# Kernel tuning notes

Measured on AMD Instinct MI355X. Metric: run time of the kernel, lower is better.

The kernel has to match this reference:

```python
import jax, jax.numpy as jnp
import numpy as np

NUM_NODES = 50000
NODE_DIM = 32
EDGE_DIM = 7
HIDDEN_DIM = 64
NUM_EDGES = 200000


def setup_inputs() -> dict:
    key = jax.random.key(0)
    ks = jax.random.split(key, 12)
    s = lambda *d: 1.0 / np.sqrt(d[0])
    return {
        "edge_index": jax.random.randint(ks[0], (2, NUM_EDGES), 0, NUM_NODES, dtype=jnp.int64)
        if jax.config.jax_enable_x64 else jax.random.randint(ks[0], (2, NUM_EDGES), 0, NUM_NODES, dtype=jnp.int32),
        "edge_attr": jax.random.normal(ks[1], (NUM_EDGES, EDGE_DIM), dtype=jnp.float32),
        # learned parameters
        "node_emb": jax.random.normal(ks[2], (NUM_NODES, NODE_DIM), dtype=jnp.float32),
        "w_nn": jax.random.normal(ks[3], (EDGE_DIM, NODE_DIM * HIDDEN_DIM), dtype=jnp.float32) * s(EDGE_DIM),
        "b_nn": jnp.zeros((NODE_DIM * HIDDEN_DIM,), dtype=jnp.float32),
        "root_w": jax.random.normal(ks[4], (NODE_DIM, HIDDEN_DIM), dtype=jnp.float32) * s(NODE_DIM),
        "conv_bias": jnp.zeros((HIDDEN_DIM,), dtype=jnp.float32),
        "w_e1": jax.random.normal(ks[5], (2 * HIDDEN_DIM + EDGE_DIM, 64), dtype=jnp.float32) * s(2 * HIDDEN_DIM + EDGE_DIM),
        "b_e1": jnp.zeros((64,), dtype=jnp.float32),
        "w_e2": jax.random.normal(ks[6], (64, 2), dtype=jnp.float32) * s(64),
        "b_e2": jnp.zeros((2,), dtype=jnp.float32),
    }


def reference(edge_index, edge_attr, node_emb, w_nn, b_nn, root_w, conv_bias,
              w_e1, b_e1, w_e2, b_e2):
    src, dst = edge_index[0], edge_index[1]
    x = node_emb  # [N, node_dim]
    # NNConv: per-edge weight matrix from edge MLP (Linear + ReLU)
    w_edge = jax.nn.relu(edge_attr @ w_nn + b_nn).reshape(-1, NODE_DIM, HIDDEN_DIM)  # [E, in, out]
    # gather source features, per-edge matmul, scatter-add to dst (aggr='add')
    msg = jnp.einsum("ei,eio->eo", x[src], w_edge)  # [E, hidden]
    agg = jax.ops.segment_sum(msg, dst, num_segments=NUM_NODES)  # [N, hidden]
    h = jax.nn.relu(agg + x @ root_w + conv_bias)  # conv root term + bias, then outer ReLU
    # edge classifier MLP
    edge_repr = jnp.concatenate([h[src], h[dst], edge_attr], axis=1)  # [E, 2H+edge_dim]
    out = jax.nn.relu(edge_repr @ w_e1 + b_e1) @ w_e2 + b_e2  # [E, 2]
    return out
```

## Files before the change

### kernel.cpp

```cpp
#include <hip/hip_runtime.h>
#include <hip/hip_bf16.h>

#define NUM_NODES 50000
#define NODE_DIM 32
#define EDGE_DIM 7
#define HIDDEN_DIM 64
#define NUM_EDGES 200000

#define INIT_BLOCKS ((NUM_NODES + 127) / 128)
#define PREP_BLOCKS ((5 * 4 * 64 * 8 + 255) / 256)

typedef __attribute__((ext_vector_type(8))) short bf16x8;
typedef __attribute__((ext_vector_type(4))) float f32x4;
typedef _Float16 h2v __attribute__((ext_vector_type(2)));

__device__ inline unsigned f2bf(float f) {
    union { float f; unsigned u; } x; x.f = f;
    return (x.u + 0x7FFFu + ((x.u >> 16) & 1u)) >> 16;
}
__device__ inline unsigned pack2bf(float a, float b) {
    return f2bf(a) | (f2bf(b) << 16);
}
__device__ inline h2v u2h(unsigned u) {
    union { unsigned u; h2v h; } c; c.u = u; return c.h;
}
__device__ inline unsigned h2u(h2v h) {
    union { h2v h; unsigned u; } c; c.h = h; return c.u;
}
__device__ inline unsigned packh2(float a, float b) {
    h2v h; h[0] = (_Float16)a; h[1] = (_Float16)b; return h2u(h);
}

__global__ __launch_bounds__(256) void k_initprep(const float* __restrict__ x,
                                                  const float* __restrict__ root_w,
                                                  const float* __restrict__ conv_bias,
                                                  const float* __restrict__ w_e1,
                                                  const float* __restrict__ b_e1,
                                                  ushort* __restrict__ aggh,
                                                  ushort* __restrict__ bfrag) {
    if (blockIdx.x >= INIT_BLOCKS) {
        int u = (blockIdx.x - INIT_BLOCKS) * blockDim.x + threadIdx.x;
        if (u < 5 * 4 * 64 * 8) {
            int j     = u & 7;
            int lane  = (u >> 3) & 63;
            int ntile = (u >> 9) & 3;
            int kstep = u >> 11;
            int k = kstep * 32 + (lane >> 4) * 8 + j;
            int o = ntile * 16 + (lane & 15);
            float v = (k < 135) ? w_e1[k * 64 + o] : ((k == 135) ? b_e1[o] : 0.f);
            bfrag[u] = (ushort)f2bf(v);
        }
        return;
    }
    __shared__ float rw[NODE_DIM * HIDDEN_DIM];
    __shared__ float cb[HIDDEN_DIM];
    __shared__ float xS[128 * NODE_DIM];
    for (int t = threadIdx.x; t < NODE_DIM * HIDDEN_DIM; t += 256) rw[t] = root_w[t];
    if (threadIdx.x < HIDDEN_DIM) cb[threadIdx.x] = conv_bias[threadIdx.x];
    const int nb = blockIdx.x * 128;
    {
        const float4* xg = (const float4*)x;
        float4* xs4 = (float4*)xS;
        #pragma unroll
        for (int r = 0; r < 4; ++r) {
            int t = r * 256 + threadIdx.x;
            int gi = nb * (NODE_DIM / 4) + t;
            xs4[t] = (gi < NUM_NODES * (NODE_DIM / 4)) ? xg[gi] : make_float4(0.f, 0.f, 0.f, 0.f);
        }
    }
    __syncthreads();
    const int lane = threadIdx.x & 63;
    const int w    = threadIdx.x >> 6;
    for (int r = 0; r < 32; ++r) {
        const int n = nb + w * 32 + r;
        if (n >= NUM_NODES) break;
        float acc = cb[lane];
        const float* xr = &xS[(w * 32 + r) * NODE_DIM];
        #pragma unroll
        for (int i = 0; i < NODE_DIM; ++i)
            acc = fmaf(xr[i], rw[i * HIDDEN_DIM + lane], acc);
        const float nbr = __shfl_down(acc, 1);
        if (!(lane & 1))
            ((unsigned*)(aggh + (size_t)n * HIDDEN_DIM))[lane >> 1] = packh2(acc, nbr);
    }
}

#define MBX 8
__global__ __launch_bounds__(512) void k_msg12(const int* __restrict__ ei,
                                               const float* __restrict__ ea,
                                               const float* __restrict__ x,
                                               const float* __restrict__ w_nn,
                                               const float* __restrict__ b_nn,
                                               ushort* __restrict__ aggh) {
    __shared__ uint4    wAu[16 * 64];
    __shared__ uint4    wBu[16 * 64];
    __shared__ unsigned xHu[8][MBX][16];
    __shared__ float    eS[8][MBX][8];
    for (int c = threadIdx.x; c < 16 * 64; c += 512) {
        const int p = c >> 6, o = c & 63;
        const int c0 = (2 * p) * 64 + o, c1 = c0 + 64;
        uint4 a, b;
        a.x = packh2(w_nn[c0],            w_nn[c1]);
        a.y = packh2(w_nn[2048 + c0],     w_nn[2048 + c1]);
        a.z = packh2(w_nn[2 * 2048 + c0], w_nn[2 * 2048 + c1]);
        a.w = packh2(w_nn[3 * 2048 + c0], w_nn[3 * 2048 + c1]);
        b.x = packh2(w_nn[4 * 2048 + c0], w_nn[4 * 2048 + c1]);
        b.y = packh2(w_nn[5 * 2048 + c0], w_nn[5 * 2048 + c1]);
        b.z = packh2(w_nn[6 * 2048 + c0], w_nn[6 * 2048 + c1]);
        b.w = packh2(b_nn[c0],            b_nn[c1]);
        wAu[c] = a; wBu[c] = b;
    }
    __syncthreads();

    const int lane   = threadIdx.x & 63;
    const int ws     = threadIdx.x >> 6;
    const int wave   = (blockIdx.x * blockDim.x + threadIdx.x) >> 6;
    const int nwaves = (gridDim.x * blockDim.x) >> 6;

    for (int e0 = wave * MBX; e0 < NUM_EDGES; e0 += nwaves * MBX) {
        int sD[MBX];
        #pragma unroll
        for (int m = 0; m < MBX; ++m)
            sD[m] = __builtin_amdgcn_readfirstlane(ei[NUM_EDGES + e0 + m]);

        {
            const int m  = lane >> 3;
            const int q4 = lane & 7;
            const int s  = ei[e0 + m];
            const float4 xv = *(const float4*)(x + (size_t)s * NODE_DIM + q4 * 4);
            xHu[ws][m][2 * q4 + 0] = packh2(xv.x, xv.y);
            xHu[ws][m][2 * q4 + 1] = packh2(xv.z, xv.w);
            if (lane < MBX * EDGE_DIM)
                eS[ws][lane / EDGE_DIM][lane % EDGE_DIM] = ea[(size_t)e0 * EDGE_DIM + lane];
        }

        float acc[MBX];
        #pragma unroll
        for (int m = 0; m < MBX; ++m) acc[m] = 0.f;

        #pragma unroll
        for (int half = 0; half < 2; ++half) {
            h2v evR[4][7];
            #pragma unroll
            for (int j = 0; j < 4; ++j) {
                const float4* e4 = (const float4*)&eS[ws][half * 4 + j][0];
                const float4 a0 = e4[0], a1 = e4[1];
                evR[j][0] = (h2v)((_Float16)a0.x);
                evR[j][1] = (h2v)((_Float16)a0.y);
                evR[j][2] = (h2v)((_Float16)a0.z);
                evR[j][3] = (h2v)((_Float16)a0.w);
                evR[j][4] = (h2v)((_Float16)a1.x);
                evR[j][5] = (h2v)((_Float16)a1.y);
                evR[j][6] = (h2v)((_Float16)a1.z);
            }

            #pragma unroll 2
            for (int p4 = 0; p4 < 4; ++p4) {
                uint4 xr[4];
                #pragma unroll
                for (int j = 0; j < 4; ++j)
                    xr[j] = *(const uint4*)&xHu[ws][half * 4 + j][p4 * 4];
                #pragma unroll
                for (int pp = 0; pp < 4; ++pp) {
                    const int p = p4 * 4 + pp;
                    const uint4 wa = wAu[p * 64 + lane];
                    const uint4 wb = wBu[p * 64 + lane];
                    #pragma unroll
                    for (int j = 0; j < 4; ++j) {
                        h2v t = u2h(wb.w);
                        t = evR[j][0] * u2h(wa.x) + t;
                        t = evR[j][1] * u2h(wa.y) + t;
                        t = evR[j][2] * u2h(wa.z) + t;
                        t = evR[j][3] * u2h(wa.w) + t;
                        t = evR[j][4] * u2h(wb.x) + t;
                        t = evR[j][5] * u2h(wb.y) + t;
                        t = evR[j][6] * u2h(wb.z) + t;
                        t = __builtin_elementwise_max(t, (h2v)((_Float16)0.f));
                        const unsigned xp = (pp == 0) ? xr[j].x : (pp == 1) ? xr[j].y
                                          : (pp == 2) ? xr[j].z : xr[j].w;
                        acc[half * 4 + j] = __builtin_amdgcn_fdot2(
                            t, u2h(xp), acc[half * 4 + j], false);
                    }
                }
            }
        }

        #pragma unroll
        for (int m = 0; m < MBX; ++m) {
            const float nbr = __shfl_down(acc[m], 1);
            if (!(lane & 1)) {
                const unsigned pk = packh2(acc[m], nbr);
                ushort* ap = aggh + (size_t)sD[m] * HIDDEN_DIM + lane;
                asm volatile("global_atomic_pk_add_f16 %0, %1, off"
                             :: "v"(ap), "v"(pk) : "memory");
            }
        }
    }
}

#define ASTRIDE 168
__global__ __launch_bounds__(256) void k_edge3(const int* __restrict__ ei,
                                               const float* __restrict__ ea,
                                               const ushort* __restrict__ aggh,
                                               const ushort* __restrict__ bfrag,
                                               const float* __restrict__ w_e2,
                                               const float* __restrict__ b_e2,
                                               float* __restrict__ out) {
    __shared__ ushort aS[64 * ASTRIDE];
    __shared__ ushort bS[5 * 4 * 64 * 8];
    __shared__ float  w2S[128];
    {
        const uint4* g = (const uint4*)bfrag;
        uint4* s = (uint4*)bS;
        for (int t = threadIdx.x; t < 1280; t += 256) s[t] = g[t];
        if (threadIdx.x < 128) w2S[threadIdx.x] = w_e2[threadIdx.x];
    }
    const int e0 = blockIdx.x * 64;
    {
        const int el = threadIdx.x >> 2;
        const int q  = threadIdx.x & 3;
        const int e  = e0 + el;
        const int src = ei[e], dst = ei[NUM_EDGES + e];
        const uint4* ps = (const uint4*)(aggh + (size_t)src * HIDDEN_DIM + q * 16);
        const uint4* pd = (const uint4*)(aggh + (size_t)dst * HIDDEN_DIM + q * 16);
        unsigned* arow = (unsigned*)(aS + el * ASTRIDE);
        #pragma unroll
        for (int i = 0; i < 2; ++i) {
            const uint4 sv = ps[i];
            const unsigned uu[4] = {sv.x, sv.y, sv.z, sv.w};
            #pragma unroll
            for (int jj = 0; jj < 4; ++jj) {
                h2v hh = u2h(uu[jj]);
                arow[q * 8 + i * 4 + jj] =
                    pack2bf(fmaxf((float)hh[0], 0.f), fmaxf((float)hh[1], 0.f));
            }
        }
        #pragma unroll
        for (int i = 0; i < 2; ++i) {
            const uint4 dv = pd[i];
            const unsigned uu[4] = {dv.x, dv.y, dv.z, dv.w};
            #pragma unroll
            for (int jj = 0; jj < 4; ++jj) {
                h2v hh = u2h(uu[jj]);
                arow[32 + q * 8 + i * 4 + jj] =
                    pack2bf(fmaxf((float)hh[0], 0.f), fmaxf((float)hh[1], 0.f));
            }
        }
        if (q == 0) {
            float ev[8];
            #pragma unroll
            for (int k = 0; k < EDGE_DIM; ++k) ev[k] = ea[e * EDGE_DIM + k];
            ev[7] = 1.0f;
            #pragma unroll
            for (int i = 0; i < 4; ++i)
                arow[64 + i] = pack2bf(ev[2 * i], ev[2 * i + 1]);
        } else {
            unsigned* z = arow + 64 + q * 4;
            z[0] = 0u; z[1] = 0u; z[2] = 0u; z[3] = 0u;
        }
    }
    __syncthreads();

    const int lane = threadIdx.x & 63;
    const int w    = threadIdx.x >> 6;
    f32x4 acc[4];
    #pragma unroll
    for (int nt = 0; nt < 4; ++nt) acc[nt] = (f32x4){0.f, 0.f, 0.f, 0.f};

    const ushort* arow = aS + (w * 16 + (lane & 15)) * ASTRIDE + (lane >> 4) * 8;
    #pragma unroll
    for (int ks = 0; ks < 5; ++ks) {
        bf16x8 af = *(const bf16x8*)(arow + ks * 32);
        #pragma unroll
        for (int nt = 0; nt < 4; ++nt) {
            bf16x8 bf = *(const bf16x8*)(bS + ((ks * 4 + nt) * 64 + lane) * 8);
            acc[nt] = __builtin_amdgcn_mfma_f32_16x16x32_bf16(af, bf, acc[nt], 0, 0, 0);
        }
    }

    float w20[4], w21[4];
    #pragma unroll
    for (int nt = 0; nt < 4; ++nt) {
        int o = nt * 16 + (lane & 15);
        w20[nt] = w2S[o * 2 + 0];
        w21[nt] = w2S[o * 2 + 1];
    }
    const float bias0 = b_e2[0], bias1 = b_e2[1];
    #pragma unroll
    for (int r = 0; r < 4; ++r) {
        float p0 = 0.f, p1 = 0.f;
        #pragma unroll
        for (int nt = 0; nt < 4; ++nt) {
            float z = fmaxf(acc[nt][r], 0.f);
            p0 = fmaf(z, w20[nt], p0);
            p1 = fmaf(z, w21[nt], p1);
        }
        #pragma unroll
        for (int off = 1; off < 16; off <<= 1) {
            p0 += __shfl_xor(p0, off);
            p1 += __shfl_xor(p1, off);
        }
        if ((lane & 15) == 0) {
            int e = e0 + w * 16 + (lane >> 4) * 4 + r;
            float2 v; v.x = p0 + bias0; v.y = p1 + bias1;
            ((float2*)out)[e] = v;
        }
    }
}

extern "C" void kernel_launch(void* const* d_in, const int* in_sizes, int n_in,
                              void* d_out, int out_size, void* d_ws, size_t ws_size,
                              hipStream_t stream) {
    const int*   ei        = (const int*)d_in[0];
    const float* edge_attr = (const float*)d_in[1];
    const float* node_emb  = (const float*)d_in[2];
    const float* w_nn      = (const float*)d_in[3];
    const float* b_nn      = (const float*)d_in[4];
    const float* root_w    = (const float*)d_in[5];
    const float* conv_bias = (const float*)d_in[6];
    const float* w_e1      = (const float*)d_in[7];
    const float* b_e1      = (const float*)d_in[8];
    const float* w_e2      = (const float*)d_in[9];
    const float* b_e2      = (const float*)d_in[10];
    float*       out       = (float*)d_out;
    ushort*      aggh      = (ushort*)d_ws;
    ushort*      bfrag     = (ushort*)((char*)d_ws + 12800000);

    k_initprep<<<INIT_BLOCKS + PREP_BLOCKS, 256, 0, stream>>>(
        node_emb, root_w, conv_bias, w_e1, b_e1, aggh, bfrag);
    k_msg12<<<1024, 512, 0, stream>>>(ei, edge_attr, node_emb, w_nn, b_nn, aggh);
    k_edge3<<<NUM_EDGES / 64, 256, 0, stream>>>(ei, edge_attr, aggh, bfrag, w_e2, b_e2, out);
}
```

Measured before the change: 118.5 us.

## Precompute replicated fp16 edge attributes and process 16 edges per wave

Measured after the change: 121.7 us. 1.03x slower.

```diff
diff --git a/kernel.cpp b/kernel.cpp
--- a/kernel.cpp
+++ b/kernel.cpp
@@ -9,6 +9,7 @@
 
 #define INIT_BLOCKS ((NUM_NODES + 127) / 128)
 #define PREP_BLOCKS ((5 * 4 * 64 * 8 + 255) / 256)
+#define EAREP_BLOCKS (NUM_EDGES * 8 / 256)
 
 typedef __attribute__((ext_vector_type(8))) short bf16x8;
 typedef __attribute__((ext_vector_type(4))) float f32x4;
@@ -36,8 +37,19 @@
                                                   const float* __restrict__ conv_bias,
                                                   const float* __restrict__ w_e1,
                                                   const float* __restrict__ b_e1,
+                                                  const float* __restrict__ ea,
                                                   ushort* __restrict__ aggh,
+                                                  unsigned* __restrict__ eaRep,
                                                   ushort* __restrict__ bfrag) {
+    if (blockIdx.x >= INIT_BLOCKS + PREP_BLOCKS) {
+        int u = (blockIdx.x - INIT_BLOCKS - PREP_BLOCKS) * blockDim.x + threadIdx.x;
+        if (u < NUM_EDGES * 8) {
+            int e = u >> 3, k = u & 7;
+            float v = (k < EDGE_DIM) ? ea[(size_t)e * EDGE_DIM + k] : 1.0f;
+            eaRep[u] = packh2(v, v);
+        }
+        return;
+    }
     if (blockIdx.x >= INIT_BLOCKS) {
         int u = (blockIdx.x - INIT_BLOCKS) * blockDim.x + threadIdx.x;
         if (u < 5 * 4 * 64 * 8) {
@@ -85,17 +97,16 @@
     }
 }
 
-#define MBX 8
-__global__ __launch_bounds__(512) void k_msg12(const int* __restrict__ ei,
-                                               const float* __restrict__ ea,
+#define MBY 16
+__global__ __launch_bounds__(512) void k_msg13(const int* __restrict__ ei,
+                                               const unsigned* __restrict__ eaRep,
                                                const float* __restrict__ x,
                                                const float* __restrict__ w_nn,
                                                const float* __restrict__ b_nn,
                                                ushort* __restrict__ aggh) {
     __shared__ uint4    wAu[16 * 64];
     __shared__ uint4    wBu[16 * 64];
-    __shared__ unsigned xHu[8][MBX][16];
-    __shared__ float    eS[8][MBX][8];
+    __shared__ unsigned xHu[8][MBY][16];
     for (int c = threadIdx.x; c < 16 * 64; c += 512) {
         const int p = c >> 6, o = c & 63;
         const int c0 = (2 * p) * 64 + o, c1 = c0 + 64;
@@ -117,41 +128,34 @@
     const int wave   = (blockIdx.x * blockDim.x + threadIdx.x) >> 6;
     const int nwaves = (gridDim.x * blockDim.x) >> 6;
 
-    for (int e0 = wave * MBX; e0 < NUM_EDGES; e0 += nwaves * MBX) {
-        int sD[MBX];
-        #pragma unroll
-        for (int m = 0; m < MBX; ++m)
+    for (int e0 = wave * MBY; e0 < NUM_EDGES; e0 += nwaves * MBY) {
+        int sD[MBY];
+        #pragma unroll
+        for (int m = 0; m < MBY; ++m)
             sD[m] = __builtin_amdgcn_readfirstlane(ei[NUM_EDGES + e0 + m]);
 
-        {
-            const int m  = lane >> 3;
-            const int q4 = lane & 7;
-            const int s  = ei[e0 + m];
+        #pragma unroll
+        for (int rep = 0; rep < 2; ++rep) {
+            const int idx = rep * 64 + lane;
+            const int m   = idx >> 3;
+            const int q4  = idx & 7;
+            const int s   = ei[e0 + m];
             const float4 xv = *(const float4*)(x + (size_t)s * NODE_DIM + q4 * 4);
             xHu[ws][m][2 * q4 + 0] = packh2(xv.x, xv.y);
             xHu[ws][m][2 * q4 + 1] = packh2(xv.z, xv.w);
-            if (lane < MBX * EDGE_DIM)
-                eS[ws][lane / EDGE_DIM][lane % EDGE_DIM] = ea[(size_t)e0 * EDGE_DIM + lane];
-        }
-
-        float acc[MBX];
-        #pragma unroll
-        for (int m = 0; m < MBX; ++m) acc[m] = 0.f;
-
-        #pragma unroll
-        for (int half = 0; half < 2; ++half) {
-            h2v evR[4][7];
+        }
+
+        float acc[MBY];
+        #pragma unroll
+        for (int m = 0; m < MBY; ++m) acc[m] = 0.f;
+
+        #pragma unroll
+        for (int q = 0; q < 4; ++q) {
+            uint4 evA[4], evB[4];
             #pragma unroll
             for (int j = 0; j < 4; ++j) {
-                const float4* e4 = (const float4*)&eS[ws][half * 4 + j][0];
-                const float4 a0 = e4[0], a1 = e4[1];
-                evR[j][0] = (h2v)((_Float16)a0.x);
-                evR[j][1] = (h2v)((_Float16)a0.y);
-                evR[j][2] = (h2v)((_Float16)a0.z);
-                evR[j][3] = (h2v)((_Float16)a0.w);
-                evR[j][4] = (h2v)((_Float16)a1.x);
-                evR[j][5] = (h2v)((_Float16)a1.y);
-                evR[j][6] = (h2v)((_Float16)a1.z);
+                const uint4* ep = (const uint4*)(eaRep + (size_t)(e0 + q * 4 + j) * 8);
+                evA[j] = ep[0]; evB[j] = ep[1];
             }
 
             #pragma unroll 2
@@ -159,7 +163,7 @@
                 uint4 xr[4];
                 #pragma unroll
                 for (int j = 0; j < 4; ++j)
-                    xr[j] = *(const uint4*)&xHu[ws][half * 4 + j][p4 * 4];
+                    xr[j] = *(const uint4*)&xHu[ws][q * 4 + j][p4 * 4];
                 #pragma unroll
                 for (int pp = 0; pp < 4; ++pp) {
                     const int p = p4 * 4 + pp;
@@ -168,25 +172,25 @@
                     #pragma unroll
                     for (int j = 0; j < 4; ++j) {
                         h2v t = u2h(wb.w);
-                        t = evR[j][0] * u2h(wa.x) + t;
-                        t = evR[j][1] * u2h(wa.y) + t;
-                        t = evR[j][2] * u2h(wa.z) + t;
-                        t = evR[j][3] * u2h(wa.w) + t;
-                        t = evR[j][4] * u2h(wb.x) + t;
-                        t = evR[j][5] * u2h(wb.y) + t;
-                        t = evR[j][6] * u2h(wb.z) + t;
+                        t = u2h(evA[j].x) * u2h(wa.x) + t;
+                        t = u2h(evA[j].y) * u2h(wa.y) + t;
+                        t = u2h(evA[j].z) * u2h(wa.z) + t;
+                        t = u2h(evA[j].w) * u2h(wa.w) + t;
+                        t = u2h(evB[j].x) * u2h(wb.x) + t;
+                        t = u2h(evB[j].y) * u2h(wb.y) + t;
+                        t = u2h(evB[j].z) * u2h(wb.z) + t;
                         t = __builtin_elementwise_max(t, (h2v)((_Float16)0.f));
                         const unsigned xp = (pp == 0) ? xr[j].x : (pp == 1) ? xr[j].y
                                           : (pp == 2) ? xr[j].z : xr[j].w;
-                        acc[half * 4 + j] = __builtin_amdgcn_fdot2(
-                            t, u2h(xp), acc[half * 4 + j], false);
+                        acc[q * 4 + j] = __builtin_amdgcn_fdot2(
+                            t, u2h(xp), acc[q * 4 + j], false);
                     }
                 }
             }
         }
 
         #pragma unroll
-        for (int m = 0; m < MBX; ++m) {
+        for (int m = 0; m < MBY; ++m) {
             const float nbr = __shfl_down(acc[m], 1);
             if (!(lane & 1)) {
                 const unsigned pk = packh2(acc[m], nbr);
@@ -324,10 +328,12 @@
     const float* b_e2      = (const float*)d_in[10];
     float*       out       = (float*)d_out;
     ushort*      aggh      = (ushort*)d_ws;
+    unsigned*    eaRep     = (unsigned*)((char*)d_ws + 6400000);
     ushort*      bfrag     = (ushort*)((char*)d_ws + 12800000);
 
-    k_initprep<<<INIT_BLOCKS + PREP_BLOCKS, 256, 0, stream>>>(
-        node_emb, root_w, conv_bias, w_e1, b_e1, aggh, bfrag);
-    k_msg12<<<1024, 512, 0, stream>>>(ei, edge_attr, node_emb, w_nn, b_nn, aggh);
+    k_initprep<<<INIT_BLOCKS + PREP_BLOCKS + EAREP_BLOCKS, 256, 0, stream>>>(
+        node_emb, root_w, conv_bias, w_e1, b_e1, edge_attr, aggh, eaRep, bfrag);
+    k_msg13<<<(NUM_EDGES / MBY + 7) / 8, 512, 0, stream>>>(
+        ei, eaRep, node_emb, w_nn, b_nn, aggh);
     k_edge3<<<NUM_EDGES / 64, 256, 0, stream>>>(ei, edge_attr, aggh, bfrag, w_e2, b_e2, out);
 }
```
